# Optimization experiments

Hardware: AMD Instinct MI355X
Metric: run time of the kernel (lower is better)

Reference implementation:

```python
import jax, jax.numpy as jnp
import numpy as np

N, E = 50000, 800000
IN_C, OUT_C, D_EMB = 64, 64, 64
NEG_SLOPE = 0.2  # GDN GraphLayer default leaky_relu slope


def setup_inputs() -> dict:
    key = jax.random.key(0)
    ks = jax.random.split(key, 9)
    return {
        "x": jax.random.normal(ks[0], (N, IN_C), jnp.float32),
        "edge_index": jax.random.randint(ks[1], (2, E), 0, N, dtype=jnp.int32),
        "embedding": jax.random.normal(ks[2], (N, D_EMB), jnp.float32),
        # learned params of GraphLayer (heads=1, concat)
        "W": jax.random.normal(ks[3], (OUT_C, IN_C), jnp.float32) * (1.0 / np.sqrt(IN_C)),
        "att_i": jax.random.normal(ks[4], (OUT_C,), jnp.float32) * 0.1,
        "att_j": jax.random.normal(ks[5], (OUT_C,), jnp.float32) * 0.1,
        "att_em_i": jax.random.normal(ks[6], (D_EMB,), jnp.float32) * 0.1,
        "att_em_j": jax.random.normal(ks[7], (D_EMB,), jnp.float32) * 0.1,
        "bias": jax.random.normal(ks[8], (OUT_C,), jnp.float32) * 0.01,
    }


def reference(x, edge_index, embedding, W, att_i, att_j, att_em_i, att_em_j, bias):
    n = x.shape[0]
    loops = jnp.arange(n, dtype=edge_index.dtype)
    src = jnp.concatenate([edge_index[0], loops])  # message source j
    dst = jnp.concatenate([edge_index[1], loops])  # message target i

    h = x @ W.T  # [N, OUT_C]
    # per-node attention scores (equivalent to cat(h, emb) . cat(att, att_em))
    s_i = h @ att_i + embedding @ att_em_i  # [N]
    s_j = h @ att_j + embedding @ att_em_j  # [N]

    alpha = s_i[dst] + s_j[src]                         # [E+N] edge logits
    alpha = jax.nn.leaky_relu(alpha, NEG_SLOPE)
    # softmax over incoming edges of each destination node
    amax = jax.ops.segment_max(alpha, dst, num_segments=n)
    ex = jnp.exp(alpha - amax[dst])
    denom = jax.ops.segment_sum(ex, dst, num_segments=n)
    alpha = ex / (denom[dst] + 1e-16)

    msg = h[src] * alpha[:, None]                       # [E+N, OUT_C]
    out = jax.ops.segment_sum(msg, dst, num_segments=n) + bias
    return jax.nn.relu(out)
```

## Files before the change

kernel.cpp:

```cpp
#include <hip/hip_runtime.h>
#include <hip/hip_bf16.h>
#include <math.h>

#define NEG_SLOPE 0.2f

#define XTA(k, r) ((k) * 64 + ((r) ^ ((((k) >> 2) & 7) << 2)))

__device__ __forceinline__ void gemm_tile(
    float* lds, int t, int tid,
    const float* __restrict__ x, const float* __restrict__ emb,
    const float* __restrict__ W,
    const float* __restrict__ att_i, const float* __restrict__ att_j,
    const float* __restrict__ att_em_i, const float* __restrict__ att_em_j,
    __hip_bfloat16* __restrict__ h, float* __restrict__ s_i,
    float* __restrict__ s_j, int N)
{
    float* XT = lds;
    float* WT = lds + 4096;

    const int rbase = t * 64;
    const int valid = min(64, N - rbase);

    #pragma unroll
    for (int i = 0; i < 4; ++i) {
        int idx = i * 256 + tid;
        int r = idx >> 4, m = idx & 15;
        float4 v = make_float4(0.f, 0.f, 0.f, 0.f);
        if (r < valid)
            v = *reinterpret_cast<const float4*>(x + (size_t)(rbase + r) * 64 + 4 * m);
        int k = 4 * m;
        XT[XTA(k + 0, r)] = v.x;
        XT[XTA(k + 1, r)] = v.y;
        XT[XTA(k + 2, r)] = v.z;
        XT[XTA(k + 3, r)] = v.w;
    }
    #pragma unroll
    for (int i = 0; i < 4; ++i) {
        int idx = i * 256 + tid;
        int c = idx >> 4, m = idx & 15;
        float4 v = *reinterpret_cast<const float4*>(W + idx * 4);
        int k = 4 * m;
        WT[XTA(k + 0, c)] = v.x;
        WT[XTA(k + 1, c)] = v.y;
        WT[XTA(k + 2, c)] = v.z;
        WT[XTA(k + 3, c)] = v.w;
    }
    __syncthreads();

    const int cg_ = tid & 15, rg = tid >> 4;
    const int c0 = cg_ * 4, r0 = rg * 4;
    float acc[4][4];
    #pragma unroll
    for (int a = 0; a < 4; ++a)
        #pragma unroll
        for (int q = 0; q < 4; ++q) acc[a][q] = 0.f;

    #pragma unroll 4
    for (int k = 0; k < 64; ++k) {
        float4 wv = *reinterpret_cast<float4*>(&WT[XTA(k, c0)]);
        float4 xa = *reinterpret_cast<float4*>(&XT[XTA(k, r0)]);
        float xs[4] = {xa.x, xa.y, xa.z, xa.w};
        float ws[4] = {wv.x, wv.y, wv.z, wv.w};
        #pragma unroll
        for (int a = 0; a < 4; ++a)
            #pragma unroll
            for (int q = 0; q < 4; ++q)
                acc[a][q] = fmaf(ws[a], xs[q], acc[a][q]);
    }

    #pragma unroll
    for (int q = 0; q < 4; ++q) {
        int r = r0 + q;
        if (r < valid) {
            union { __hip_bfloat16 p[4]; uint2 u; } pk;
            pk.p[0] = __float2bfloat16(acc[0][q]);
            pk.p[1] = __float2bfloat16(acc[1][q]);
            pk.p[2] = __float2bfloat16(acc[2][q]);
            pk.p[3] = __float2bfloat16(acc[3][q]);
            *reinterpret_cast<uint2*>(h + (size_t)(rbase + r) * 64 + c0) = pk.u;
        }
    }

    float ai[4], aj[4];
    #pragma unroll
    for (int a = 0; a < 4; ++a) { ai[a] = att_i[c0 + a]; aj[a] = att_j[c0 + a]; }

    __syncthreads();
    float* RED_I = lds;
    float* RED_J = lds + 1088;
    float* EMT   = lds + 4096;

    #pragma unroll
    for (int q = 0; q < 4; ++q) {
        int r = r0 + q;
        float pi = acc[0][q]*ai[0] + acc[1][q]*ai[1] + acc[2][q]*ai[2] + acc[3][q]*ai[3];
        float pj = acc[0][q]*aj[0] + acc[1][q]*aj[1] + acc[2][q]*aj[2] + acc[3][q]*aj[3];
        RED_I[r * 17 + cg_] = pi;
        RED_J[r * 17 + cg_] = pj;
    }
    #pragma unroll
    for (int i = 0; i < 4; ++i) {
        int idx = i * 256 + tid;
        int r = idx >> 4, m = idx & 15;
        float4 v = make_float4(0.f, 0.f, 0.f, 0.f);
        if (r < valid)
            v = *reinterpret_cast<const float4*>(emb + (size_t)(rbase + r) * 64 + 4 * m);
        int k = 4 * m;
        EMT[XTA(k + 0, r)] = v.x;
        EMT[XTA(k + 1, r)] = v.y;
        EMT[XTA(k + 2, r)] = v.z;
        EMT[XTA(k + 3, r)] = v.w;
    }
    __syncthreads();

    if (tid < 64 && tid < valid) {
        float ri = 0.f, rj = 0.f;
        #pragma unroll
        for (int j = 0; j < 16; ++j) {
            ri += RED_I[tid * 17 + j];
            rj += RED_J[tid * 17 + j];
        }
        float ei = 0.f, ej = 0.f;
        #pragma unroll 16
        for (int k = 0; k < 64; ++k) {
            float ev = EMT[XTA(k, tid)];
            ei = fmaf(ev, att_em_i[k], ei);
            ej = fmaf(ev, att_em_j[k], ej);
        }
        s_i[rbase + tid] = ri + ei;
        s_j[rbase + tid] = rj + ej;
    }
}

__global__ __launch_bounds__(256) void k_gemm_scatter(
    const float* __restrict__ x, const float* __restrict__ emb,
    const float* __restrict__ W,
    const float* __restrict__ att_i, const float* __restrict__ att_j,
    const float* __restrict__ att_em_i, const float* __restrict__ att_em_j,
    const int* __restrict__ srcA, const int* __restrict__ dstA,
    int* __restrict__ cursor, unsigned short* __restrict__ csr,
    __hip_bfloat16* __restrict__ h, float* __restrict__ s_i,
    float* __restrict__ s_j, int N, int E, int GB, int sh, int nchunks)
{
    __shared__ float lds[8192];
    const int tid = threadIdx.x;

    if ((int)blockIdx.x >= GB) {
        const int b2    = blockIdx.x - GB;
        const int oct   = b2 & 7;
        const int chunk = b2 >> 3;
        const int npos  = nchunks * 256;
        const int E4    = E >> 2;
        const int4* d4p = reinterpret_cast<const int4*>(dstA);
        const int4* s4p = reinterpret_cast<const int4*>(srcA);
        for (int p = chunk * 256 + tid; p < E4; p += npos) {
            int4 d4 = d4p[p];
            int4 s4 = s4p[p];
            int dd[4] = {d4.x, d4.y, d4.z, d4.w};
            int ss[4] = {s4.x, s4.y, s4.z, s4.w};
            #pragma unroll
            for (int i = 0; i < 4; ++i) {
                if ((dd[i] >> sh) == oct) {
                    int pos = atomicAdd(&cursor[dd[i]], 1);
                    if (pos < 64)
                        csr[(size_t)dd[i] * 64 + pos] = (unsigned short)ss[i];
                }
            }
        }
        for (int e = E4 * 4 + chunk * 256 + tid; e < E; e += npos) {
            int d = dstA[e];
            if ((d >> sh) == oct) {
                int pos = atomicAdd(&cursor[d], 1);
                if (pos < 64)
                    csr[(size_t)d * 64 + pos] = (unsigned short)srcA[e];
            }
        }
        return;
    }

    gemm_tile(lds, blockIdx.x, tid, x, emb, W, att_i, att_j,
              att_em_i, att_em_j, h, s_i, s_j, N);
}

__global__ __launch_bounds__(256) void k_aggregate(
    const __hip_bfloat16* __restrict__ h, const float* __restrict__ s_i,
    const float* __restrict__ s_j, const int* __restrict__ cursor,
    const unsigned short* __restrict__ csr, const float* __restrict__ bias,
    float* __restrict__ out, int N)
{
    const int lane = threadIdx.x & 63;
    const int node = (blockIdx.x * blockDim.x + threadIdx.x) >> 6;
    if (node >= N) return;

    int deg_e = cursor[node];
    deg_e = (deg_e > 63) ? 63 : deg_e;
    const int degT = deg_e + 1;
    const float si = s_i[node];

    int s = node;
    if (lane < deg_e) s = csr[(size_t)node * 64 + lane];
    float ex = 0.f;
    if (lane < degT) {
        float a = si + s_j[s];
        a = (a > 0.f) ? a : NEG_SLOPE * a;
        ex = __expf(a);
    }
    float l = ex;
    #pragma unroll
    for (int off = 32; off > 0; off >>= 1) l += __shfl_xor(l, off);

    const int half = lane >> 5;
    const int hc   = lane & 31;
    const unsigned* hp = reinterpret_cast<const unsigned*>(h);
    float ax = 0.f, ay = 0.f;

    const int nPairs = (degT + 1) >> 1;
    for (int base = 0; base < nPairs; base += 16) {
        const int cnt = min(16, nPairs - base);
        unsigned ubuf[16];
        float    ebuf[16];
        #pragma unroll
        for (int p = 0; p < 16; ++p) {
            if (p < cnt) {
                int jj = 2 * (base + p) + half;
                int jc = (jj < degT) ? jj : (degT - 1);
                float e = __shfl(ex, jc);
                int   t = __shfl(s, jc);
                if (jj >= degT) e = 0.f;
                ebuf[p] = e;
                ubuf[p] = hp[(size_t)t * 32 + hc];
            }
        }
        #pragma unroll
        for (int p = 0; p < 16; ++p) {
            if (p < cnt) {
                ax = fmaf(ebuf[p], __uint_as_float(ubuf[p] << 16), ax);
                ay = fmaf(ebuf[p], __uint_as_float(ubuf[p] & 0xffff0000u), ay);
            }
        }
    }

    ax += __shfl_xor(ax, 32);
    ay += __shfl_xor(ay, 32);

    if (half == 0) {
        float inv = 1.f / (l + 1e-16f);
        float2 bv = *reinterpret_cast<const float2*>(bias + 2 * hc);
        float2 o;
        o.x = fmaxf(ax * inv + bv.x, 0.f);
        o.y = fmaxf(ay * inv + bv.y, 0.f);
        *reinterpret_cast<float2*>(out + (size_t)node * 64 + 2 * hc) = o;
    }
}

extern "C" void kernel_launch(void* const* d_in, const int* in_sizes, int n_in,
                              void* d_out, int out_size, void* d_ws, size_t ws_size,
                              hipStream_t stream) {
    const float* x        = (const float*)d_in[0];
    const int*   ei       = (const int*)  d_in[1];
    const float* emb      = (const float*)d_in[2];
    const float* W        = (const float*)d_in[3];
    const float* att_i    = (const float*)d_in[4];
    const float* att_j    = (const float*)d_in[5];
    const float* att_em_i = (const float*)d_in[6];
    const float* att_em_j = (const float*)d_in[7];
    const float* bias     = (const float*)d_in[8];
    float* out = (float*)d_out;

    const int N = in_sizes[0] / 64;
    const int E = in_sizes[1] / 2;
    const int* e_src = ei;
    const int* e_dst = ei + E;

    char* ws = (char*)d_ws;
    __hip_bfloat16* h = (__hip_bfloat16*)ws;  ws += (size_t)N * 64 * 2;
    float* s_i     = (float*)ws;  ws += (size_t)N * 4;
    float* s_j     = (float*)ws;  ws += (size_t)N * 4;
    int*   cursor  = (int*)ws;    ws += (size_t)N * 4;
    unsigned short* csr = (unsigned short*)ws;  ws += (size_t)N * 64 * 2;

    int sh = 0;
    while ((1 << sh) < N) ++sh;
    sh -= 3;

    const int GB = (N + 63) / 64;
    const int NCHUNK = 256;

    hipMemsetAsync(cursor, 0, (size_t)N * 4, stream);
    k_gemm_scatter<<<GB + NCHUNK * 8, 256, 0, stream>>>(
        x, emb, W, att_i, att_j, att_em_i, att_em_j,
        e_src, e_dst, cursor, csr, h, s_i, s_j, N, E, GB, sh, NCHUNK);
    k_aggregate<<<(N * 64 + 255) / 256, 256, 0, stream>>>(h, s_i, s_j, cursor,
                                                          csr, bias, out, N);
}
```

Before: 154.7 us.

## Gather four neighbors per iteration via LDS edge table and skip unneeded src loads

The aggregation kernel now writes each lane's (exp weight, source index) pair into a per-wave LDS table. Each quarter-wave then handles one neighbor per iteration, loading 8 bytes (4 bf16 channels) per lane instead of 4, so every iteration covers four neighbors rather than two. The intent is fewer gather iterations and fewer shuffles, at the cost of a reduction across quarter-waves at the end. The CSR build kernel also loads the source vector only when at least one destination in the int4 falls in its octant, cutting redundant source reads. Rows in the LDS table beyond degT are read but get a zero weight, and no barrier is needed because each wave only touches its own row.

Result: no change. 153.5 us, median of 2 (-0.8%).

```diff
diff --git a/kernel.cpp b/kernel.cpp
--- a/kernel.cpp
+++ b/kernel.cpp
@@ -155,16 +155,18 @@
         const int4* s4p = reinterpret_cast<const int4*>(srcA);
         for (int p = chunk * 256 + tid; p < E4; p += npos) {
             int4 d4 = d4p[p];
-            int4 s4 = s4p[p];
-            int dd[4] = {d4.x, d4.y, d4.z, d4.w};
-            int ss[4] = {s4.x, s4.y, s4.z, s4.w};
-            #pragma unroll
-            for (int i = 0; i < 4; ++i) {
-                if ((dd[i] >> sh) == oct) {
-                    int pos = atomicAdd(&cursor[dd[i]], 1);
-                    if (pos < 64)
-                        csr[(size_t)dd[i] * 64 + pos] = (unsigned short)ss[i];
-                }
+            bool m0 = (d4.x >> sh) == oct, m1 = (d4.y >> sh) == oct;
+            bool m2 = (d4.z >> sh) == oct, m3 = (d4.w >> sh) == oct;
+            if (m0 | m1 | m2 | m3) {
+                int4 s4 = s4p[p];
+                if (m0) { int pos = atomicAdd(&cursor[d4.x], 1);
+                          if (pos < 64) csr[(size_t)d4.x * 64 + pos] = (unsigned short)s4.x; }
+                if (m1) { int pos = atomicAdd(&cursor[d4.y], 1);
+                          if (pos < 64) csr[(size_t)d4.y * 64 + pos] = (unsigned short)s4.y; }
+                if (m2) { int pos = atomicAdd(&cursor[d4.z], 1);
+                          if (pos < 64) csr[(size_t)d4.z * 64 + pos] = (unsigned short)s4.z; }
+                if (m3) { int pos = atomicAdd(&cursor[d4.w], 1);
+                          if (pos < 64) csr[(size_t)d4.w * 64 + pos] = (unsigned short)s4.w; }
             }
         }
         for (int e = E4 * 4 + chunk * 256 + tid; e < E; e += npos) {
@@ -188,8 +190,11 @@
     const unsigned short* __restrict__ csr, const float* __restrict__ bias,
     float* __restrict__ out, int N)
 {
-    const int lane = threadIdx.x & 63;
-    const int node = (blockIdx.x * blockDim.x + threadIdx.x) >> 6;
+    __shared__ uint2 tbl[4][64];
+    const int tid  = threadIdx.x;
+    const int lane = tid & 63;
+    const int wid  = tid >> 6;
+    const int node = (blockIdx.x * blockDim.x + tid) >> 6;
     if (node >= N) return;
 
     int deg_e = cursor[node];
@@ -209,47 +214,40 @@
     #pragma unroll
     for (int off = 32; off > 0; off >>= 1) l += __shfl_xor(l, off);
 
-    const int half = lane >> 5;
-    const int hc   = lane & 31;
-    const unsigned* hp = reinterpret_cast<const unsigned*>(h);
-    float ax = 0.f, ay = 0.f;
-
-    const int nPairs = (degT + 1) >> 1;
-    for (int base = 0; base < nPairs; base += 16) {
-        const int cnt = min(16, nPairs - base);
-        unsigned ubuf[16];
-        float    ebuf[16];
-        #pragma unroll
-        for (int p = 0; p < 16; ++p) {
-            if (p < cnt) {
-                int jj = 2 * (base + p) + half;
-                int jc = (jj < degT) ? jj : (degT - 1);
-                float e = __shfl(ex, jc);
-                int   t = __shfl(s, jc);
-                if (jj >= degT) e = 0.f;
-                ebuf[p] = e;
-                ubuf[p] = hp[(size_t)t * 32 + hc];
-            }
-        }
-        #pragma unroll
-        for (int p = 0; p < 16; ++p) {
-            if (p < cnt) {
-                ax = fmaf(ebuf[p], __uint_as_float(ubuf[p] << 16), ax);
-                ay = fmaf(ebuf[p], __uint_as_float(ubuf[p] & 0xffff0000u), ay);
-            }
-        }
-    }
-
-    ax += __shfl_xor(ax, 32);
-    ay += __shfl_xor(ay, 32);
-
-    if (half == 0) {
+    tbl[wid][lane] = make_uint2(__float_as_uint(ex), (unsigned)s);
+
+    const int q  = lane >> 4;
+    const int c4 = lane & 15;
+    const uint2* hp2 = reinterpret_cast<const uint2*>(h);
+    float a0 = 0.f, a1 = 0.f, a2 = 0.f, a3 = 0.f;
+
+    const int iters = (degT + 3) >> 2;
+    #pragma unroll 2
+    for (int it = 0; it < iters; ++it) {
+        uint2 rec = tbl[wid][4 * it + q];
+        float e = __uint_as_float(rec.x);
+        int   t = (int)rec.y;
+        uint2 u = hp2[(size_t)t * 16 + c4];
+        a0 = fmaf(e, __uint_as_float(u.x << 16), a0);
+        a1 = fmaf(e, __uint_as_float(u.x & 0xffff0000u), a1);
+        a2 = fmaf(e, __uint_as_float(u.y << 16), a2);
+        a3 = fmaf(e, __uint_as_float(u.y & 0xffff0000u), a3);
+    }
+
+    a0 += __shfl_xor(a0, 16); a0 += __shfl_xor(a0, 32);
+    a1 += __shfl_xor(a1, 16); a1 += __shfl_xor(a1, 32);
+    a2 += __shfl_xor(a2, 16); a2 += __shfl_xor(a2, 32);
+    a3 += __shfl_xor(a3, 16); a3 += __shfl_xor(a3, 32);
+
+    if (lane < 16) {
         float inv = 1.f / (l + 1e-16f);
-        float2 bv = *reinterpret_cast<const float2*>(bias + 2 * hc);
-        float2 o;
-        o.x = fmaxf(ax * inv + bv.x, 0.f);
-        o.y = fmaxf(ay * inv + bv.y, 0.f);
-        *reinterpret_cast<float2*>(out + (size_t)node * 64 + 2 * hc) = o;
+        float4 bv = *reinterpret_cast<const float4*>(bias + 4 * c4);
+        float4 o;
+        o.x = fmaxf(a0 * inv + bv.x, 0.f);
+        o.y = fmaxf(a1 * inv + bv.y, 0.f);
+        o.z = fmaxf(a2 * inv + bv.z, 0.f);
+        o.w = fmaxf(a3 * inv + bv.w, 0.f);
+        *reinterpret_cast<float4*>(out + (size_t)node * 64 + 4 * c4) = o;
     }
 }
 
```
